# Optimization experiments

Measured on AMD Instinct MI355X. Metric: run time of the kernel, lower is better.

Reference implementation:

```python
import jax, jax.numpy as jnp
import numpy as np

B, H, L, D = 2, 16, 1024, 64
R, E = 16, 4  # num_relations, rank


def setup_inputs() -> dict:
    key = jax.random.key(0)
    k1, k2, k3, k4, k5 = jax.random.split(key, 5)
    Q = jax.random.normal(k1, (B, H, L, D), jnp.float32)
    K = jax.random.normal(k2, (B, H, L, D), jnp.float32)
    relation_ids = jax.random.randint(k3, (B, L, L), 0, R, jnp.int32)
    # Original inits A1/A2 to zeros (identity A); use small random values so the
    # low-rank relation-specific term is exercised nontrivially.
    A1 = jax.random.normal(k4, (R, H, D, E), jnp.float32) * 0.02
    A2 = jax.random.normal(k5, (R, H, E, D), jnp.float32) * 0.02
    return {"Q": Q, "K": K, "relation_ids": relation_ids, "A1": A1, "A2": A2}


def reference(Q, K, relation_ids, A1, A2):
    # A_r = A1_r @ A2_r + I, so score[b,h,l,m] = Q.K^T + (Q A1_r)(A2_r K^T)
    # with r = relation_ids[b,l,m]. Entries whose relation id is outside
    # [0, R) are never accumulated in the original loop -> masked to 0.
    num_rel = A1.shape[0]
    rank = A1.shape[-1]
    base = jnp.einsum('bhld,bhmd->bhlm', Q, K)                 # identity part
    u = jnp.einsum('bhld,rhde->bhlre', Q, A1)                  # (B,H,L,R,E) small
    v = jnp.einsum('bhmd,rhed->bhmre', K, A2)                  # (B,H,M,R,E) small
    idx = jnp.clip(relation_ids, 0, num_rel - 1)
    # gather per-(l,m) relation's query projection: (B,H,L,L,E)
    ug = jnp.take_along_axis(u, idx[:, None, :, :, None], axis=3)
    # gather per-(l,m) relation's key projection: (B,H,L,M,E)
    vg = jnp.take_along_axis(v[:, :, None], idx[:, None, :, :, None, None], axis=4)[..., 0, :]
    low = jnp.sum(ug * vg, axis=-1)
    valid = ((relation_ids >= 0) & (relation_ids < num_rel))[:, None]
    return (base + low) * valid.astype(base.dtype)
```

## Files before the change

### kernel.cpp

```cpp
#include <hip/hip_runtime.h>
#include <hip/hip_bf16.h>
#include <stdint.h>

#define Bsz 2
#define Hn  16
#define Ln  1024
#define Dn  64
#define Rn  16
#define En  4

typedef short short8 __attribute__((ext_vector_type(8)));
typedef float f32x4  __attribute__((ext_vector_type(4)));

__device__ __forceinline__ unsigned short f32_to_bf16_rne(float f) {
    union { float f; uint32_t u; } x; x.f = f;
    uint32_t u = x.u;
    u += 0x7FFFu + ((u >> 16) & 1u);
    return (unsigned short)(u >> 16);
}

__device__ __forceinline__ float bf16_to_f32(unsigned short s) {
    union { uint32_t u; float f; } x; x.u = ((uint32_t)s) << 16;
    return x.f;
}

__global__ __launch_bounds__(256) void uv_kernel(
    const float* __restrict__ Q, const float* __restrict__ K,
    const float* __restrict__ A1, const float* __restrict__ A2,
    unsigned short* __restrict__ ws_u, unsigned short* __restrict__ ws_v)
{
    __shared__ float Xs[16 * 68];
    __shared__ float Ah[16 * 65 * 4];

    const int tid = threadIdx.x;
    const int bh  = blockIdx.y;
    const int h   = bh & 15;
    const int l0  = blockIdx.x * 16;
    const int isV = blockIdx.z;

    const float* X = (isV ? K : Q) + (size_t)bh * Ln * Dn;

    {
        const int row = tid >> 4, c4 = tid & 15;
        const float4 v = *(const float4*)&X[(size_t)(l0 + row) * Dn + c4 * 4];
        *(float4*)&Xs[row * 68 + c4 * 4] = v;
    }
    if (!isV) {
        #pragma unroll
        for (int i = 0; i < 4; ++i) {
            const int p = tid + i * 256;
            const int r = p >> 6, d = p & 63;
            const float4 v = *(const float4*)&A1[(((size_t)r * Hn + h) * Dn + d) * En];
            *(float4*)&Ah[(r * 65 + d) * 4] = v;
        }
    } else {
        #pragma unroll
        for (int i = 0; i < 4; ++i) {
            const int p = tid + i * 256;
            const int r = p >> 6, d = p & 63;
            float4 v;
            v.x = A2[(((size_t)r * Hn + h) * En + 0) * Dn + d];
            v.y = A2[(((size_t)r * Hn + h) * En + 1) * Dn + d];
            v.z = A2[(((size_t)r * Hn + h) * En + 2) * Dn + d];
            v.w = A2[(((size_t)r * Hn + h) * En + 3) * Dn + d];
            *(float4*)&Ah[(r * 65 + d) * 4] = v;
        }
    }
    __syncthreads();

    const int li = tid >> 4, r = tid & 15;
    float ax = 0.f, ay = 0.f, az = 0.f, aw = 0.f;
    #pragma unroll
    for (int d = 0; d < Dn; ++d) {
        const float x = Xs[li * 68 + d];
        const float4 a = *(const float4*)&Ah[(r * 65 + d) * 4];
        ax += x * a.x; ay += x * a.y; az += x * a.z; aw += x * a.w;
    }
    unsigned short* dst = (isV ? ws_v : ws_u);
    ushort4 o;
    o.x = f32_to_bf16_rne(ax); o.y = f32_to_bf16_rne(ay);
    o.z = f32_to_bf16_rne(az); o.w = f32_to_bf16_rne(aw);
    *(ushort4*)&dst[((size_t)bh * Ln + l0 + li) * 64 + r * 4] = o;
}

__global__ __launch_bounds__(256, 5) void score_kernel(
    const float* __restrict__ Q, const float* __restrict__ K,
    const int* __restrict__ rid,
    const unsigned short* __restrict__ ws_u, const unsigned short* __restrict__ ws_v,
    float* __restrict__ out)
{
    __shared__ unsigned short Ks[64 * 72];
    __shared__ unsigned short us[64 * 68];
    __shared__ unsigned short vs[64 * 68];

    const int tid = threadIdx.x;
    const int bh  = blockIdx.z;
    const int b   = bh >> 4;
    const int m0  = blockIdx.x * 64;
    const int l0  = blockIdx.y * 64;

    const int w    = tid >> 6;
    const int lane = tid & 63;
    const int quad = lane >> 4;
    const int ln   = lane & 15;

    const size_t qkBase = (size_t)bh * Ln * Dn;
    const size_t uvBase = (size_t)bh * Ln * 64;

    float4 qa[2][2];
    #pragma unroll
    for (int s = 0; s < 2; ++s) {
        const float* qp = &Q[qkBase + (size_t)(l0 + w * 16 + ln) * Dn + s * 32 + quad * 8];
        qa[s][0] = *(const float4*)qp;
        qa[s][1] = *(const float4*)(qp + 4);
    }

    int ridv[16];
    {
        const size_t ridRow0 = ((size_t)b * Ln + l0 + w * 16 + quad * 4) * Ln + m0 + ln;
        #pragma unroll
        for (int t = 0; t < 4; ++t)
            #pragma unroll
            for (int reg = 0; reg < 4; ++reg)
                ridv[t * 4 + reg] = rid[ridRow0 + (size_t)reg * Ln + t * 16];
    }

    #pragma unroll
    for (int i = 0; i < 4; ++i) {
        const int p = tid + i * 256;
        const int row = p >> 4, c4 = p & 15;
        const float4 k = *(const float4*)&K[qkBase + (size_t)(m0 + row) * Dn + c4 * 4];
        ushort4 kb;
        kb.x = f32_to_bf16_rne(k.x); kb.y = f32_to_bf16_rne(k.y);
        kb.z = f32_to_bf16_rne(k.z); kb.w = f32_to_bf16_rne(k.w);
        *(ushort4*)&Ks[row * 72 + c4 * 4] = kb;
        const ushort4 u = *(const ushort4*)&ws_u[uvBase + (size_t)(l0 + row) * 64 + c4 * 4];
        const ushort4 v = *(const ushort4*)&ws_v[uvBase + (size_t)(m0 + row) * 64 + c4 * 4];
        *(ushort4*)&us[row * 68 + c4 * 4] = u;
        *(ushort4*)&vs[row * 68 + c4 * 4] = v;
    }

    short8 aF[2];
    #pragma unroll
    for (int s = 0; s < 2; ++s) {
        #pragma unroll
        for (int j = 0; j < 4; ++j) {
            aF[s][j]     = (short)f32_to_bf16_rne(qa[s][0][j]);
            aF[s][4 + j] = (short)f32_to_bf16_rne(qa[s][1][j]);
        }
    }
    __syncthreads();

    f32x4 acc[4];
    #pragma unroll
    for (int t = 0; t < 4; ++t) { f32x4 z = {0.f, 0.f, 0.f, 0.f}; acc[t] = z; }

    #pragma unroll
    for (int s = 0; s < 2; ++s) {
        #pragma unroll
        for (int t = 0; t < 4; ++t) {
            const short8 bF = *(const short8*)&Ks[(t * 16 + ln) * 72 + s * 32 + quad * 8];
            acc[t] = __builtin_amdgcn_mfma_f32_16x16x32_bf16(aF[s], bF, acc[t], 0, 0, 0);
        }
    }

    #pragma unroll
    for (int t = 0; t < 4; ++t) {
        const int m_local = t * 16 + ln;
        const int m = m0 + m_local;
        #pragma unroll
        for (int reg = 0; reg < 4; ++reg) {
            const int l_local = w * 16 + quad * 4 + reg;
            const int l = l0 + l_local;
            const int rv = ridv[t * 4 + reg];
            const bool valid = (rv >= 0) && (rv < Rn);
            const int r = valid ? rv : 0;
            const ushort4 uu = *(const ushort4*)&us[l_local * 68 + r * 4];
            const ushort4 vv = *(const ushort4*)&vs[m_local * 68 + r * 4];
            const float low = bf16_to_f32(uu.x) * bf16_to_f32(vv.x)
                            + bf16_to_f32(uu.y) * bf16_to_f32(vv.y)
                            + bf16_to_f32(uu.z) * bf16_to_f32(vv.z)
                            + bf16_to_f32(uu.w) * bf16_to_f32(vv.w);
            const float res = valid ? (acc[t][reg] + low) : 0.f;
            __builtin_nontemporal_store(res, &out[((size_t)bh * Ln + l) * Ln + m]);
        }
    }
}

extern "C" void kernel_launch(void* const* d_in, const int* in_sizes, int n_in,
                              void* d_out, int out_size, void* d_ws, size_t ws_size,
                              hipStream_t stream) {
    const float* Q   = (const float*)d_in[0];
    const float* K   = (const float*)d_in[1];
    const int*   rid = (const int*)d_in[2];
    const float* A1  = (const float*)d_in[3];
    const float* A2  = (const float*)d_in[4];
    float* out = (float*)d_out;

    unsigned short* ws_u = (unsigned short*)d_ws;
    unsigned short* ws_v = ws_u + (size_t)Bsz * Hn * Ln * 64;

    uv_kernel<<<dim3(Ln / 16, Bsz * Hn, 2), 256, 0, stream>>>(Q, K, A1, A2, ws_u, ws_v);
    score_kernel<<<dim3(Ln / 64, Ln / 64, Bsz * Hn), 256, 0, stream>>>(Q, K, rid, ws_u, ws_v, out);
}
```

Measured before the change: 199.5 us.

## Precompute bf16 Q/K in prepass and stage tiles via direct global-to-LDS loads

The uv prepass now also writes bf16 copies of Q and K to workspace, with K stored in an XOR-swizzled layout per 64-row tile. The score kernel drops fp32 Q/K reads and their per-tile conversion. It loads K, u and v tiles with global_load_lds straight into unpadded shared memory and reads the swizzled K for bank-conflict-free MFMA operands. Occupancy hint goes from 5 to 6, at the cost of extra workspace writes in the prepass.

```diff
diff --git a/kernel.cpp b/kernel.cpp
--- a/kernel.cpp
+++ b/kernel.cpp
@@ -24,10 +24,17 @@
     return x.f;
 }
 
+__device__ __forceinline__ void gload_lds16(const void* g, void* l) {
+    __builtin_amdgcn_global_load_lds(
+        (const __attribute__((address_space(1))) unsigned int*)g,
+        (__attribute__((address_space(3))) unsigned int*)l, 16, 0, 0);
+}
+
 __global__ __launch_bounds__(256) void uv_kernel(
     const float* __restrict__ Q, const float* __restrict__ K,
     const float* __restrict__ A1, const float* __restrict__ A2,
-    unsigned short* __restrict__ ws_u, unsigned short* __restrict__ ws_v)
+    unsigned short* __restrict__ ws_u, unsigned short* __restrict__ ws_v,
+    unsigned short* __restrict__ ws_q, unsigned short* __restrict__ ws_k)
 {
     __shared__ float Xs[16 * 68];
     __shared__ float Ah[16 * 65 * 4];
@@ -68,6 +75,22 @@
     }
     __syncthreads();
 
+    if (tid < 128) {
+        const int row = tid >> 3, ci = tid & 7;
+        const float* src = &Xs[row * 68 + ci * 8];
+        short8 o;
+        #pragma unroll
+        for (int j = 0; j < 8; ++j) o[j] = (short)f32_to_bf16_rne(src[j]);
+        const int grow = l0 + row;
+        if (!isV) {
+            *(short8*)&ws_q[((size_t)bh * Ln + grow) * 64 + ci * 8] = o;
+        } else {
+            const unsigned a  = (unsigned)(((grow & 63) * 128) + ci * 16);
+            const unsigned sw = a ^ (((unsigned)(grow & 7)) << 4);
+            *(short8*)((char*)ws_k + ((size_t)bh * Ln + (grow & ~63)) * 128 + sw) = o;
+        }
+    }
+
     const int li = tid >> 4, r = tid & 15;
     float ax = 0.f, ay = 0.f, az = 0.f, aw = 0.f;
     #pragma unroll
@@ -83,15 +106,15 @@
     *(ushort4*)&dst[((size_t)bh * Ln + l0 + li) * 64 + r * 4] = o;
 }
 
-__global__ __launch_bounds__(256, 5) void score_kernel(
-    const float* __restrict__ Q, const float* __restrict__ K,
+__global__ __launch_bounds__(256, 6) void score_kernel(
     const int* __restrict__ rid,
     const unsigned short* __restrict__ ws_u, const unsigned short* __restrict__ ws_v,
+    const unsigned short* __restrict__ ws_q, const unsigned short* __restrict__ ws_k,
     float* __restrict__ out)
 {
-    __shared__ unsigned short Ks[64 * 72];
-    __shared__ unsigned short us[64 * 68];
-    __shared__ unsigned short vs[64 * 68];
+    __shared__ unsigned short Ks[64 * 64];
+    __shared__ unsigned short us[64 * 64];
+    __shared__ unsigned short vs[64 * 64];
 
     const int tid = threadIdx.x;
     const int bh  = blockIdx.z;
@@ -104,16 +127,24 @@
     const int quad = lane >> 4;
     const int ln   = lane & 15;
 
-    const size_t qkBase = (size_t)bh * Ln * Dn;
-    const size_t uvBase = (size_t)bh * Ln * 64;
-
-    float4 qa[2][2];
-    #pragma unroll
-    for (int s = 0; s < 2; ++s) {
-        const float* qp = &Q[qkBase + (size_t)(l0 + w * 16 + ln) * Dn + s * 32 + quad * 8];
-        qa[s][0] = *(const float4*)qp;
-        qa[s][1] = *(const float4*)(qp + 4);
-    }
+    {
+        const char* kSrc = (const char*)ws_k + ((size_t)bh * Ln + m0) * 128;
+        const char* uSrc = (const char*)ws_u + ((size_t)bh * Ln + l0) * 128;
+        const char* vSrc = (const char*)ws_v + ((size_t)bh * Ln + m0) * 128;
+        const int o0 = w * 2048 + lane * 16;
+        const int o1 = o0 + 1024;
+        gload_lds16(kSrc + o0, (char*)Ks + o0);
+        gload_lds16(kSrc + o1, (char*)Ks + o1);
+        gload_lds16(uSrc + o0, (char*)us + o0);
+        gload_lds16(uSrc + o1, (char*)us + o1);
+        gload_lds16(vSrc + o0, (char*)vs + o0);
+        gload_lds16(vSrc + o1, (char*)vs + o1);
+    }
+
+    short8 aF[2];
+    #pragma unroll
+    for (int s = 0; s < 2; ++s)
+        aF[s] = *(const short8*)&ws_q[((size_t)bh * Ln + l0 + w * 16 + ln) * 64 + s * 32 + quad * 8];
 
     int ridv[16];
     {
@@ -125,41 +156,20 @@
                 ridv[t * 4 + reg] = rid[ridRow0 + (size_t)reg * Ln + t * 16];
     }
 
-    #pragma unroll
-    for (int i = 0; i < 4; ++i) {
-        const int p = tid + i * 256;
-        const int row = p >> 4, c4 = p & 15;
-        const float4 k = *(const float4*)&K[qkBase + (size_t)(m0 + row) * Dn + c4 * 4];
-        ushort4 kb;
-        kb.x = f32_to_bf16_rne(k.x); kb.y = f32_to_bf16_rne(k.y);
-        kb.z = f32_to_bf16_rne(k.z); kb.w = f32_to_bf16_rne(k.w);
-        *(ushort4*)&Ks[row * 72 + c4 * 4] = kb;
-        const ushort4 u = *(const ushort4*)&ws_u[uvBase + (size_t)(l0 + row) * 64 + c4 * 4];
-        const ushort4 v = *(const ushort4*)&ws_v[uvBase + (size_t)(m0 + row) * 64 + c4 * 4];
-        *(ushort4*)&us[row * 68 + c4 * 4] = u;
-        *(ushort4*)&vs[row * 68 + c4 * 4] = v;
-    }
-
-    short8 aF[2];
+    __syncthreads();
+
+    f32x4 acc[4];
+    #pragma unroll
+    for (int t = 0; t < 4; ++t) { f32x4 z = {0.f, 0.f, 0.f, 0.f}; acc[t] = z; }
+
+    const int  xorv = (ln & 7) << 4;
+    const char* KsB = (const char*)Ks;
     #pragma unroll
     for (int s = 0; s < 2; ++s) {
-        #pragma unroll
-        for (int j = 0; j < 4; ++j) {
-            aF[s][j]     = (short)f32_to_bf16_rne(qa[s][0][j]);
-            aF[s][4 + j] = (short)f32_to_bf16_rne(qa[s][1][j]);
-        }
-    }
-    __syncthreads();
-
-    f32x4 acc[4];
-    #pragma unroll
-    for (int t = 0; t < 4; ++t) { f32x4 z = {0.f, 0.f, 0.f, 0.f}; acc[t] = z; }
-
-    #pragma unroll
-    for (int s = 0; s < 2; ++s) {
+        const int co = (s * 64 + quad * 16) ^ xorv;
         #pragma unroll
         for (int t = 0; t < 4; ++t) {
-            const short8 bF = *(const short8*)&Ks[(t * 16 + ln) * 72 + s * 32 + quad * 8];
+            const short8 bF = *(const short8*)(KsB + t * 2048 + ln * 128 + co);
             acc[t] = __builtin_amdgcn_mfma_f32_16x16x32_bf16(aF[s], bF, acc[t], 0, 0, 0);
         }
     }
@@ -175,8 +185,8 @@
             const int rv = ridv[t * 4 + reg];
             const bool valid = (rv >= 0) && (rv < Rn);
             const int r = valid ? rv : 0;
-            const ushort4 uu = *(const ushort4*)&us[l_local * 68 + r * 4];
-            const ushort4 vv = *(const ushort4*)&vs[m_local * 68 + r * 4];
+            const ushort4 uu = *(const ushort4*)&us[l_local * 64 + r * 4];
+            const ushort4 vv = *(const ushort4*)&vs[m_local * 64 + r * 4];
             const float low = bf16_to_f32(uu.x) * bf16_to_f32(vv.x)
                             + bf16_to_f32(uu.y) * bf16_to_f32(vv.y)
                             + bf16_to_f32(uu.z) * bf16_to_f32(vv.z)
@@ -197,9 +207,14 @@
     const float* A2  = (const float*)d_in[4];
     float* out = (float*)d_out;
 
+    const size_t seg = (size_t)Bsz * Hn * Ln * 64;
     unsigned short* ws_u = (unsigned short*)d_ws;
-    unsigned short* ws_v = ws_u + (size_t)Bsz * Hn * Ln * 64;
-
-    uv_kernel<<<dim3(Ln / 16, Bsz * Hn, 2), 256, 0, stream>>>(Q, K, A1, A2, ws_u, ws_v);
-    score_kernel<<<dim3(Ln / 64, Ln / 64, Bsz * Hn), 256, 0, stream>>>(Q, K, rid, ws_u, ws_v, out);
-}
+    unsigned short* ws_v = ws_u + seg;
+    unsigned short* ws_q = ws_v + seg;
+    unsigned short* ws_k = ws_q + seg;
+
+    uv_kernel<<<dim3(Ln / 16, Bsz * Hn, 2), 256, 0, stream>>>(Q, K, A1, A2,
+                                                              ws_u, ws_v, ws_q, ws_k);
+    score_kernel<<<dim3(Ln / 64, Ln / 64, Bsz * Hn), 256, 0, stream>>>(rid, ws_u, ws_v,
+                                                                       ws_q, ws_k, out);
+}
```

Result: faster. 192.5 us (-3.5%).
